# Kernel optimization log

Hardware: AMD Instinct MI355X
Metric: run time of the kernel (lower is better)

## Reference

```python
import jax, jax.numpy as jnp
import numpy as np

DIM = 2048
THRESH = 0.33

def _ternary(w):
    # sign() with dead zone: {-1, 0, +1}; detached from grad (matches torch.no_grad)
    return jax.lax.stop_gradient(jnp.where(jnp.abs(w) < THRESH, 0.0, jnp.sign(w)))

def _bitlinear(x, w, b):
    # F.linear(x, ternary_w, bias): x @ ternary_w.T + b
    return jnp.einsum('bsd,od->bso', x, _ternary(w)) + b

def setup_inputs() -> dict:
    key = jax.random.key(0)
    ks = jax.random.split(key, 6)
    B, S, D = 8, 2048, DIM
    x = jax.random.normal(ks[0], (B, S, D), dtype=jnp.float32)
    h_prev = jax.random.normal(ks[1], (B, S, D), dtype=jnp.float32)
    # BitLinear reset_parameters: uniform(-1, 1); bias zeros
    wf = jax.random.uniform(ks[2], (D, D), minval=-1.0, maxval=1.0, dtype=jnp.float32)
    wc = jax.random.uniform(ks[3], (D, D), minval=-1.0, maxval=1.0, dtype=jnp.float32)
    wg = jax.random.uniform(ks[4], (D, D), minval=-1.0, maxval=1.0, dtype=jnp.float32)
    wo = jax.random.uniform(ks[5], (D, D), minval=-1.0, maxval=1.0, dtype=jnp.float32)
    bf = jnp.zeros((D,), dtype=jnp.float32)
    bc = jnp.zeros((D,), dtype=jnp.float32)
    bg = jnp.zeros((D,), dtype=jnp.float32)
    bo = jnp.zeros((D,), dtype=jnp.float32)
    return {"x": x, "h_prev": h_prev, "wf": wf, "bf": bf, "wc": wc, "bc": bc,
            "wg": wg, "bg": bg, "wo": wo, "bo": bo}

def reference(x, h_prev, wf, bf, wc, bc, wg, bg, wo, bo):
    f = jax.nn.sigmoid(_bitlinear(x, wf, bf))
    c = jax.nn.silu(_bitlinear(x, wc, bc))
    h = f * h_prev + (1.0 - f) * c
    g = jax.nn.sigmoid(_bitlinear(x, wg, bg))
    o = _bitlinear(g * h, wo, bo)
    return (o, h)
```

## Files before the change

### kernel.cpp

```cpp
#include <hip/hip_runtime.h>
#include <hip/hip_bf16.h>
#include <cstdint>

#define DIM   2048
#define MROWS 16384
#define NT    32

typedef __bf16 bf16x8 __attribute__((ext_vector_type(8)));
typedef float  f32x4  __attribute__((ext_vector_type(4)));
typedef unsigned short u16;
typedef unsigned int   u32;

#define BARRIER() asm volatile("s_barrier" ::: "memory")
#define WAITVM(N) asm volatile("s_waitcnt vmcnt(" #N ")" ::: "memory")


__device__ __forceinline__ u16 ternary_bits(float w) {
    u32 u = __float_as_uint(w);
    u16 s = (u16)((u >> 16) & 0x8000u);
    return (__builtin_fabsf(w) < 0.33f) ? (u16)0 : (u16)(0x3F80u | s);
}

__device__ __forceinline__ u16 f2bf_rne(float f) {
    u32 u = __float_as_uint(f);
    u32 r = (u + 0x7FFFu + ((u >> 16) & 1u)) >> 16;
    return (u16)r;
}

__device__ __forceinline__ void gload16(const void* g, void* l) {
    __builtin_amdgcn_global_load_lds(
        (const __attribute__((address_space(1))) void*)g,
        (__attribute__((address_space(3))) void*)l,
        16, 0, 0);
}


__global__ void prep_weights(const float* __restrict__ wf, const float* __restrict__ wc,
                             const float* __restrict__ wg, const float* __restrict__ wo,
                             u16* __restrict__ out) {
    const float* srcs[4] = {wf, wc, wg, wo};
    const float* src = srcs[blockIdx.y];
    u16* dst = out + (size_t)blockIdx.y * (DIM * DIM);
    int e = (blockIdx.x * 256 + threadIdx.x) * 8;
    float4 v0 = *(const float4*)(src + e);
    float4 v1 = *(const float4*)(src + e + 4);
    ushort4 o0, o1;
    o0.x = ternary_bits(v0.x); o0.y = ternary_bits(v0.y);
    o0.z = ternary_bits(v0.z); o0.w = ternary_bits(v0.w);
    o1.x = ternary_bits(v1.x); o1.y = ternary_bits(v1.y);
    o1.z = ternary_bits(v1.z); o1.w = ternary_bits(v1.w);
    *(ushort4*)(dst + e)     = o0;
    *(ushort4*)(dst + e + 4) = o1;
}

__global__ void cast_x(const float* __restrict__ x, u16* __restrict__ xb) {
    size_t e = ((size_t)blockIdx.x * 256 + threadIdx.x) * 8;
    float4 v0 = *(const float4*)(x + e);
    float4 v1 = *(const float4*)(x + e + 4);
    ushort4 o0, o1;
    o0.x = f2bf_rne(v0.x); o0.y = f2bf_rne(v0.y);
    o0.z = f2bf_rne(v0.z); o0.w = f2bf_rne(v0.w);
    o1.x = f2bf_rne(v1.x); o1.y = f2bf_rne(v1.y);
    o1.z = f2bf_rne(v1.z); o1.w = f2bf_rne(v1.w);
    *(ushort4*)(xb + e)     = o0;
    *(ushort4*)(xb + e + 4) = o1;
}


__global__ __launch_bounds__(512) void gemm1(
    const u16* __restrict__ xb,
    const u16* __restrict__ wt,
    const float* __restrict__ bfv_, const float* __restrict__ bcv_, const float* __restrict__ bgv_,
    const float* __restrict__ hprev,
    float* __restrict__ hout,
    u16* __restrict__ gh)
{
    __shared__ __align__(16) u16 sA[2][2][128 * 32];
    __shared__ __align__(16) u16 sB[2][2][3][128 * 32];

    const int tid  = threadIdx.x;
    const int lane = tid & 63;
    const int wave = tid >> 6;
    const int wr   = wave >> 2;
    const int wcq  = wave & 3;

    const int bid  = blockIdx.x;
    const int swz  = (bid & 7) * 256 + (bid >> 3);
    const int brow = (swz & 127) * 128;
    const int bcol = (swz >> 7) * 128;

    const int row512 = tid >> 2;
    const int gc4    = (tid & 3) ^ ((tid >> 3) & 3);
    const int ldst   = tid * 8;

    const int fr  = lane & 15;
    const int hi  = lane >> 4;
    const int csw = (hi ^ ((fr >> 1) & 3)) * 8;

    f32x4 acc0[3][4] = {};
    f32x4 acc1[3][4] = {};

    const u16* aSrc  = xb + (size_t)(brow + row512) * DIM;
    const u16* bSrc0 = wt + (size_t)(bcol + row512) * DIM;
    const size_t WSTRIDE = (size_t)DIM * DIM;

    auto issueA = [&](int buf, int kt, int ks) {
        gload16(aSrc + kt + ks * 32 + gc4 * 8, (u16*)&sA[buf][ks][ldst]);
    };
    auto issueB = [&](int buf, int kt, int g, int ks) {
        gload16(bSrc0 + (size_t)g * WSTRIDE + kt + ks * 32 + gc4 * 8,
                (u16*)&sB[buf][ks][g][ldst]);
    };

    auto rdA = [&](const u16* lA, int ks, bf16x8 (&a)[4]) {
        #pragma unroll
        for (int mi = 0; mi < 4; ++mi)
            a[mi] = *(const bf16x8*)(lA + ks * 4096 + (wr * 64 + mi * 16 + fr) * 32 + csw);
    };
    auto rdB = [&](const u16* lB, int ks, int ni, bf16x8 (&b)[3]) {
        #pragma unroll
        for (int g = 0; g < 3; ++g)
            b[g] = *(const bf16x8*)(lB + ks * 12288 + g * 4096 + (wcq * 32 + ni * 16 + fr) * 32 + csw);
    };
    auto domfma = [&](bf16x8 (&a)[4], bf16x8 (&b)[3], f32x4 (&c)[3][4]) {
        __builtin_amdgcn_s_setprio(1);
        #pragma unroll
        for (int g = 0; g < 3; ++g)
            #pragma unroll
            for (int mi = 0; mi < 4; ++mi)
                c[g][mi] = __builtin_amdgcn_mfma_f32_16x16x32_bf16(a[mi], b[g], c[g][mi], 0, 0, 0);
        __builtin_amdgcn_s_setprio(0);
    };

    issueA(0, 0, 0); issueB(0, 0, 0, 0);
    issueB(0, 0, 1, 0); issueB(0, 0, 2, 0);
    issueA(0, 0, 1); issueB(0, 0, 0, 1);
    issueB(0, 0, 1, 1); issueB(0, 0, 2, 1);
    WAITVM(0);
    BARRIER();

    #pragma unroll 1
    for (int t = 0; t < NT - 1; ++t) {
        const u16* lA = &sA[t & 1][0][0];
        const u16* lB = &sB[t & 1][0][0][0];
        const int nb = (t + 1) & 1;
        const int kn = (t + 1) * 64;
        bf16x8 a[4], b[3];
        rdA(lA, 0, a); rdB(lB, 0, 0, b);
        issueA(nb, kn, 0); issueB(nb, kn, 0, 0);
        BARRIER();
        domfma(a, b, acc0);
        BARRIER();
        rdB(lB, 0, 1, b);
        issueB(nb, kn, 1, 0); issueB(nb, kn, 2, 0);
        WAITVM(4);
        BARRIER();
        domfma(a, b, acc1);
        BARRIER();
        rdA(lA, 1, a); rdB(lB, 1, 0, b);
        issueA(nb, kn, 1); issueB(nb, kn, 0, 1);
        BARRIER();
        domfma(a, b, acc0);
        BARRIER();
        rdB(lB, 1, 1, b);
        issueB(nb, kn, 1, 1); issueB(nb, kn, 2, 1);
        WAITVM(4);
        BARRIER();
        domfma(a, b, acc1);
        BARRIER();
    }
    {
        const u16* lA = &sA[1][0][0];
        const u16* lB = &sB[1][0][0][0];
        bf16x8 a[4], b[3];
        rdA(lA, 0, a); rdB(lB, 0, 0, b);
        BARRIER(); domfma(a, b, acc0); BARRIER();
        rdB(lB, 0, 1, b);
        WAITVM(0);
        BARRIER(); domfma(a, b, acc1); BARRIER();
        rdA(lA, 1, a); rdB(lB, 1, 0, b);
        BARRIER(); domfma(a, b, acc0); BARRIER();
        rdB(lB, 1, 1, b);
        domfma(a, b, acc1);
    }

    auto epi = [&](int ni, f32x4 (&c)[3][4]) {
        const int col = bcol + wcq * 32 + ni * 16 + fr;
        const float bfv = bfv_[col], bcv = bcv_[col], bgv = bgv_[col];
        #pragma unroll
        for (int mi = 0; mi < 4; ++mi) {
            #pragma unroll
            for (int j = 0; j < 4; ++j) {
                const int row = brow + wr * 64 + mi * 16 + hi * 4 + j;
                const size_t idx = (size_t)row * DIM + col;
                float pf = c[0][mi][j] + bfv;
                float pc = c[1][mi][j] + bcv;
                float pg = c[2][mi][j] + bgv;
                float f  = 1.f / (1.f + __expf(-pf));
                float cc = pc / (1.f + __expf(-pc));
                float g  = 1.f / (1.f + __expf(-pg));
                float h  = f * hprev[idx] + (1.f - f) * cc;
                hout[idx] = h;
                gh[idx] = f2bf_rne(g * h);
            }
        }
    };
    epi(0, acc0);
    epi(1, acc1);
}


__global__ __launch_bounds__(512) void gemm2(
    const u16* __restrict__ gh,
    const u16* __restrict__ wot,
    const float* __restrict__ bov_,
    float* __restrict__ oout)
{
    __shared__ __align__(16) u16 sA[2][2][128 * 32];
    __shared__ __align__(16) u16 sB[2][2][256 * 32];

    const int tid  = threadIdx.x;
    const int lane = tid & 63;
    const int wave = tid >> 6;
    const int wr   = wave >> 2;
    const int wcq  = wave & 3;

    const int bid  = blockIdx.x;
    const int swz  = (bid & 7) * 128 + (bid >> 3);
    const int brow = (swz & 127) * 128;
    const int bcol = (swz >> 7) * 256;

    const int row512 = tid >> 2;
    const int gc4    = (tid & 3) ^ ((tid >> 3) & 3);
    const int ldst   = tid * 8;

    const int fr  = lane & 15;
    const int hi  = lane >> 4;
    const int csw = (hi ^ ((fr >> 1) & 3)) * 8;

    f32x4 accL[4][2] = {};
    f32x4 accH[4][2] = {};

    const u16* aSrc  = gh  + (size_t)(brow + row512) * DIM;
    const u16* bSrcL = wot + (size_t)(bcol + row512) * DIM;
    const u16* bSrcH = wot + (size_t)(bcol + 128 + row512) * DIM;

    auto issueA = [&](int buf, int kt, int ks) {
        gload16(aSrc + kt + ks * 32 + gc4 * 8, (u16*)&sA[buf][ks][ldst]);
    };
    auto issueBlo = [&](int buf, int kt, int ks) {
        gload16(bSrcL + kt + ks * 32 + gc4 * 8, (u16*)&sB[buf][ks][ldst]);
    };
    auto issueBhi = [&](int buf, int kt, int ks) {
        gload16(bSrcH + kt + ks * 32 + gc4 * 8, (u16*)&sB[buf][ks][4096 + ldst]);
    };

    auto rdA = [&](const u16* lA, int ks, bf16x8 (&a)[4]) {
        #pragma unroll
        for (int mi = 0; mi < 4; ++mi)
            a[mi] = *(const bf16x8*)(lA + ks * 4096 + (wr * 64 + mi * 16 + fr) * 32 + csw);
    };
    auto rdB2 = [&](const u16* lB, int ks, int nbase, bf16x8 (&b)[2]) {
        #pragma unroll
        for (int jn = 0; jn < 2; ++jn)
            b[jn] = *(const bf16x8*)(lB + ks * 8192 + (wcq * 64 + (nbase + jn) * 16 + fr) * 32 + csw);
    };
    auto domfma2 = [&](bf16x8 (&a)[4], bf16x8 (&b)[2], f32x4 (&c)[4][2]) {
        __builtin_amdgcn_s_setprio(1);
        #pragma unroll
        for (int jn = 0; jn < 2; ++jn)
            #pragma unroll
            for (int mi = 0; mi < 4; ++mi)
                c[mi][jn] = __builtin_amdgcn_mfma_f32_16x16x32_bf16(a[mi], b[jn], c[mi][jn], 0, 0, 0);
        __builtin_amdgcn_s_setprio(0);
    };

    issueA(0, 0, 0); issueBlo(0, 0, 0);
    issueBhi(0, 0, 0); issueA(0, 0, 1);
    issueBlo(0, 0, 1);
    issueBhi(0, 0, 1);
    WAITVM(0);
    BARRIER();

    #pragma unroll 1
    for (int t = 0; t < NT - 1; ++t) {
        const u16* lA = &sA[t & 1][0][0];
        const u16* lB = &sB[t & 1][0][0];
        const int nb = (t + 1) & 1;
        const int kn = (t + 1) * 64;
        bf16x8 a[4], b[2];
        rdA(lA, 0, a); rdB2(lB, 0, 0, b);
        issueA(nb, kn, 0); issueBlo(nb, kn, 0);
        BARRIER();
        domfma2(a, b, accL);
        BARRIER();
        rdB2(lB, 0, 2, b);
        issueBhi(nb, kn, 0); issueA(nb, kn, 1);
        WAITVM(4);
        BARRIER();
        domfma2(a, b, accH);
        BARRIER();
        rdA(lA, 1, a); rdB2(lB, 1, 0, b);
        issueBlo(nb, kn, 1);
        BARRIER();
        domfma2(a, b, accL);
        BARRIER();
        rdB2(lB, 1, 2, b);
        issueBhi(nb, kn, 1);
        WAITVM(3);
        BARRIER();
        domfma2(a, b, accH);
        BARRIER();
    }
    {
        const u16* lA = &sA[1][0][0];
        const u16* lB = &sB[1][0][0];
        bf16x8 a[4], b[2];
        rdA(lA, 0, a); rdB2(lB, 0, 0, b);
        BARRIER(); domfma2(a, b, accL); BARRIER();
        rdB2(lB, 0, 2, b);
        WAITVM(0);
        BARRIER(); domfma2(a, b, accH); BARRIER();
        rdA(lA, 1, a); rdB2(lB, 1, 0, b);
        BARRIER(); domfma2(a, b, accL); BARRIER();
        rdB2(lB, 1, 2, b);
        domfma2(a, b, accH);
    }

    auto epi2 = [&](int nbase, f32x4 (&c)[4][2]) {
        #pragma unroll
        for (int jn = 0; jn < 2; ++jn) {
            const int col = bcol + wcq * 64 + (nbase + jn) * 16 + fr;
            const float bov = bov_[col];
            #pragma unroll
            for (int mi = 0; mi < 4; ++mi)
                #pragma unroll
                for (int j = 0; j < 4; ++j)
                    oout[(size_t)(brow + wr * 64 + mi * 16 + hi * 4 + j) * DIM + col] = c[mi][jn][j] + bov;
        }
    };
    epi2(0, accL);
    epi2(2, accH);
}

extern "C" void kernel_launch(void* const* d_in, const int* in_sizes, int n_in,
                              void* d_out, int out_size, void* d_ws, size_t ws_size,
                              hipStream_t stream) {
    const float* x  = (const float*)d_in[0];
    const float* hp = (const float*)d_in[1];
    const float* wf = (const float*)d_in[2];
    const float* bf = (const float*)d_in[3];
    const float* wc = (const float*)d_in[4];
    const float* bc = (const float*)d_in[5];
    const float* wg = (const float*)d_in[6];
    const float* bg = (const float*)d_in[7];
    const float* wo = (const float*)d_in[8];
    const float* bo = (const float*)d_in[9];

    float* o_out = (float*)d_out;
    float* h_out = o_out + (size_t)MROWS * DIM;

    u16* w_t  = (u16*)d_ws;
    u16* x_bf = (u16*)((char*)d_ws + 33554432);
    u16* gh   = (u16*)((char*)d_ws + 100663296);

    prep_weights<<<dim3(2048, 4), 256, 0, stream>>>(wf, wc, wg, wo, w_t);
    cast_x<<<dim3(16384), 256, 0, stream>>>(x, x_bf);
    gemm1<<<dim3(2048), 512, 0, stream>>>(x_bf, w_t, bf, bc, bg, hp, h_out, gh);
    gemm2<<<dim3(1024), 512, 0, stream>>>(gh, w_t + 3 * (size_t)DIM * DIM, bo, o_out);
}
```

Measured before the change: 801.7 us.

## Double M-tile to 256 rows and switch GEMMs to triple-buffered K32 pipeline

Both GEMMs now compute 256-row output tiles instead of 128, so each wave holds 8 M-fragments and B tiles are reused across twice as many rows, halving the grid size. The K loop moves from double-buffered 64-wide steps to a three-stage ring of 32-wide LDS buffers with rotating offsets, prefetching two stages ahead. The aim is less global and LDS traffic per MFMA and better latency hiding. In exchange it doubles accumulator registers (gemm1 holds 48 f32x4 accumulators), which may cut occupancy or cause spills, and it leaves fewer blocks per CU to cover the tail.

```diff
diff --git a/kernel.cpp b/kernel.cpp
--- a/kernel.cpp
+++ b/kernel.cpp
@@ -4,7 +4,7 @@
 
 #define DIM   2048
 #define MROWS 16384
-#define NT    32
+#define NH    64
 
 typedef __bf16 bf16x8 __attribute__((ext_vector_type(8)));
 typedef float  f32x4  __attribute__((ext_vector_type(4)));
@@ -75,8 +75,7 @@
     float* __restrict__ hout,
     u16* __restrict__ gh)
 {
-    __shared__ __align__(16) u16 sA[2][2][128 * 32];
-    __shared__ __align__(16) u16 sB[2][2][3][128 * 32];
+    __shared__ __align__(16) u16 lds[3 * 20480];
 
     const int tid  = threadIdx.x;
     const int lane = tid & 63;
@@ -85,113 +84,98 @@
     const int wcq  = wave & 3;
 
     const int bid  = blockIdx.x;
-    const int swz  = (bid & 7) * 256 + (bid >> 3);
-    const int brow = (swz & 127) * 128;
-    const int bcol = (swz >> 7) * 128;
-
-    const int row512 = tid >> 2;
-    const int gc4    = (tid & 3) ^ ((tid >> 3) & 3);
-    const int ldst   = tid * 8;
+    const int swz  = (bid & 7) * 128 + (bid >> 3);
+    const int brow = (swz & 63) * 256;
+    const int bcol = (swz >> 6) * 128;
+
+    const int srow = tid >> 2;
+    const int gc4  = (tid & 3) ^ ((tid >> 3) & 3);
+    const int ldst = tid * 8;
 
     const int fr  = lane & 15;
     const int hi  = lane >> 4;
     const int csw = (hi ^ ((fr >> 1) & 3)) * 8;
 
-    f32x4 acc0[3][4] = {};
-    f32x4 acc1[3][4] = {};
-
-    const u16* aSrc  = xb + (size_t)(brow + row512) * DIM;
-    const u16* bSrc0 = wt + (size_t)(bcol + row512) * DIM;
-    const size_t WSTRIDE = (size_t)DIM * DIM;
-
-    auto issueA = [&](int buf, int kt, int ks) {
-        gload16(aSrc + kt + ks * 32 + gc4 * 8, (u16*)&sA[buf][ks][ldst]);
-    };
-    auto issueB = [&](int buf, int kt, int g, int ks) {
-        gload16(bSrc0 + (size_t)g * WSTRIDE + kt + ks * 32 + gc4 * 8,
-                (u16*)&sB[buf][ks][g][ldst]);
-    };
-
-    auto rdA = [&](const u16* lA, int ks, bf16x8 (&a)[4]) {
-        #pragma unroll
-        for (int mi = 0; mi < 4; ++mi)
-            a[mi] = *(const bf16x8*)(lA + ks * 4096 + (wr * 64 + mi * 16 + fr) * 32 + csw);
-    };
-    auto rdB = [&](const u16* lB, int ks, int ni, bf16x8 (&b)[3]) {
+    f32x4 acc0[3][8] = {};
+    f32x4 acc1[3][8] = {};
+
+    const u16* aSrc0 = xb + (size_t)(brow + srow) * DIM;
+    const u16* aSrc1 = xb + (size_t)(brow + 128 + srow) * DIM;
+    const u16* bSrcB = wt + (size_t)(bcol + srow) * DIM;
+    const size_t WST = (size_t)DIM * DIM;
+
+    auto issueA = [&](int so, int k0) {
+        gload16(aSrc0 + k0 + gc4 * 8, (u16*)&lds[so + ldst]);
+        gload16(aSrc1 + k0 + gc4 * 8, (u16*)&lds[so + 4096 + ldst]);
+    };
+    auto issueB = [&](int so, int k0, int g) {
+        gload16(bSrcB + (size_t)g * WST + k0 + gc4 * 8,
+                (u16*)&lds[so + 8192 + g * 4096 + ldst]);
+    };
+
+    auto rdA = [&](int so, bf16x8 (&a)[8]) {
+        #pragma unroll
+        for (int mi = 0; mi < 8; ++mi)
+            a[mi] = *(const bf16x8*)(&lds[so + (wr * 128 + mi * 16 + fr) * 32 + csw]);
+    };
+    auto rdB = [&](int so, int ni, bf16x8 (&b)[3]) {
         #pragma unroll
         for (int g = 0; g < 3; ++g)
-            b[g] = *(const bf16x8*)(lB + ks * 12288 + g * 4096 + (wcq * 32 + ni * 16 + fr) * 32 + csw);
-    };
-    auto domfma = [&](bf16x8 (&a)[4], bf16x8 (&b)[3], f32x4 (&c)[3][4]) {
+            b[g] = *(const bf16x8*)(&lds[so + 8192 + g * 4096 + (wcq * 32 + ni * 16 + fr) * 32 + csw]);
+    };
+    auto domfma = [&](bf16x8 (&a)[8], bf16x8 (&b)[3], f32x4 (&c)[3][8]) {
         __builtin_amdgcn_s_setprio(1);
         #pragma unroll
         for (int g = 0; g < 3; ++g)
             #pragma unroll
-            for (int mi = 0; mi < 4; ++mi)
+            for (int mi = 0; mi < 8; ++mi)
                 c[g][mi] = __builtin_amdgcn_mfma_f32_16x16x32_bf16(a[mi], b[g], c[g][mi], 0, 0, 0);
         __builtin_amdgcn_s_setprio(0);
     };
 
-    issueA(0, 0, 0); issueB(0, 0, 0, 0);
-    issueB(0, 0, 1, 0); issueB(0, 0, 2, 0);
-    issueA(0, 0, 1); issueB(0, 0, 0, 1);
-    issueB(0, 0, 1, 1); issueB(0, 0, 2, 1);
+    int so0 = 0, so1 = 20480, so2 = 40960;
+
+    issueA(so0, 0); issueB(so0, 0, 0); issueB(so0, 0, 1); issueB(so0, 0, 2);
+    issueA(so1, 32); issueB(so1, 32, 0); issueB(so1, 32, 1); issueB(so1, 32, 2);
+    WAITVM(5);
+    BARRIER();
+
+    bf16x8 a[8], b[3];
+    #pragma unroll 1
+    for (int h = 0; h < NH - 2; ++h) {
+        const int kn = (h + 2) * 32;
+        rdA(so0, a); rdB(so0, 0, b);
+        issueA(so2, kn); issueB(so2, kn, 0);
+        BARRIER();
+        domfma(a, b, acc0);
+        BARRIER();
+        rdB(so0, 1, b);
+        issueB(so2, kn, 1); issueB(so2, kn, 2);
+        WAITVM(5);
+        BARRIER();
+        domfma(a, b, acc1);
+        BARRIER();
+        int t = so0; so0 = so1; so1 = so2; so2 = t;
+    }
+    rdA(so0, a); rdB(so0, 0, b);
+    BARRIER(); domfma(a, b, acc0); BARRIER();
+    rdB(so0, 1, b);
     WAITVM(0);
-    BARRIER();
-
-    #pragma unroll 1
-    for (int t = 0; t < NT - 1; ++t) {
-        const u16* lA = &sA[t & 1][0][0];
-        const u16* lB = &sB[t & 1][0][0][0];
-        const int nb = (t + 1) & 1;
-        const int kn = (t + 1) * 64;
-        bf16x8 a[4], b[3];
-        rdA(lA, 0, a); rdB(lB, 0, 0, b);
-        issueA(nb, kn, 0); issueB(nb, kn, 0, 0);
-        BARRIER();
-        domfma(a, b, acc0);
-        BARRIER();
-        rdB(lB, 0, 1, b);
-        issueB(nb, kn, 1, 0); issueB(nb, kn, 2, 0);
-        WAITVM(4);
-        BARRIER();
-        domfma(a, b, acc1);
-        BARRIER();
-        rdA(lA, 1, a); rdB(lB, 1, 0, b);
-        issueA(nb, kn, 1); issueB(nb, kn, 0, 1);
-        BARRIER();
-        domfma(a, b, acc0);
-        BARRIER();
-        rdB(lB, 1, 1, b);
-        issueB(nb, kn, 1, 1); issueB(nb, kn, 2, 1);
-        WAITVM(4);
-        BARRIER();
-        domfma(a, b, acc1);
-        BARRIER();
-    }
-    {
-        const u16* lA = &sA[1][0][0];
-        const u16* lB = &sB[1][0][0][0];
-        bf16x8 a[4], b[3];
-        rdA(lA, 0, a); rdB(lB, 0, 0, b);
-        BARRIER(); domfma(a, b, acc0); BARRIER();
-        rdB(lB, 0, 1, b);
-        WAITVM(0);
-        BARRIER(); domfma(a, b, acc1); BARRIER();
-        rdA(lA, 1, a); rdB(lB, 1, 0, b);
-        BARRIER(); domfma(a, b, acc0); BARRIER();
-        rdB(lB, 1, 1, b);
-        domfma(a, b, acc1);
-    }
-
-    auto epi = [&](int ni, f32x4 (&c)[3][4]) {
+    BARRIER(); domfma(a, b, acc1); BARRIER();
+    { int t = so0; so0 = so1; so1 = so2; so2 = t; }
+    rdA(so0, a); rdB(so0, 0, b);
+    domfma(a, b, acc0);
+    rdB(so0, 1, b);
+    domfma(a, b, acc1);
+
+    auto epi = [&](int ni, f32x4 (&c)[3][8]) {
         const int col = bcol + wcq * 32 + ni * 16 + fr;
         const float bfv = bfv_[col], bcv = bcv_[col], bgv = bgv_[col];
         #pragma unroll
-        for (int mi = 0; mi < 4; ++mi) {
+        for (int mi = 0; mi < 8; ++mi) {
             #pragma unroll
             for (int j = 0; j < 4; ++j) {
-                const int row = brow + wr * 64 + mi * 16 + hi * 4 + j;
+                const int row = brow + wr * 128 + mi * 16 + hi * 4 + j;
                 const size_t idx = (size_t)row * DIM + col;
                 float pf = c[0][mi][j] + bfv;
                 float pc = c[1][mi][j] + bcv;
@@ -199,9 +183,9 @@
                 float f  = 1.f / (1.f + __expf(-pf));
                 float cc = pc / (1.f + __expf(-pc));
                 float g  = 1.f / (1.f + __expf(-pg));
-                float h  = f * hprev[idx] + (1.f - f) * cc;
-                hout[idx] = h;
-                gh[idx] = f2bf_rne(g * h);
+                float hh = f * hprev[idx] + (1.f - f) * cc;
+                hout[idx] = hh;
+                gh[idx] = f2bf_rne(g * hh);
             }
         }
     };
@@ -216,8 +200,7 @@
     const float* __restrict__ bov_,
     float* __restrict__ oout)
 {
-    __shared__ __align__(16) u16 sA[2][2][128 * 32];
-    __shared__ __align__(16) u16 sB[2][2][256 * 32];
+    __shared__ __align__(16) u16 lds[3 * 16384];
 
     const int tid  = threadIdx.x;
     const int lane = tid & 63;
@@ -226,117 +209,100 @@
     const int wcq  = wave & 3;
 
     const int bid  = blockIdx.x;
-    const int swz  = (bid & 7) * 128 + (bid >> 3);
-    const int brow = (swz & 127) * 128;
-    const int bcol = (swz >> 7) * 256;
-
-    const int row512 = tid >> 2;
-    const int gc4    = (tid & 3) ^ ((tid >> 3) & 3);
-    const int ldst   = tid * 8;
+    const int swz  = (bid & 7) * 64 + (bid >> 3);
+    const int brow = (swz & 63) * 256;
+    const int bcol = (swz >> 6) * 256;
+
+    const int srow = tid >> 2;
+    const int gc4  = (tid & 3) ^ ((tid >> 3) & 3);
+    const int ldst = tid * 8;
 
     const int fr  = lane & 15;
     const int hi  = lane >> 4;
     const int csw = (hi ^ ((fr >> 1) & 3)) * 8;
 
-    f32x4 accL[4][2] = {};
-    f32x4 accH[4][2] = {};
-
-    const u16* aSrc  = gh  + (size_t)(brow + row512) * DIM;
-    const u16* bSrcL = wot + (size_t)(bcol + row512) * DIM;
-    const u16* bSrcH = wot + (size_t)(bcol + 128 + row512) * DIM;
-
-    auto issueA = [&](int buf, int kt, int ks) {
-        gload16(aSrc + kt + ks * 32 + gc4 * 8, (u16*)&sA[buf][ks][ldst]);
-    };
-    auto issueBlo = [&](int buf, int kt, int ks) {
-        gload16(bSrcL + kt + ks * 32 + gc4 * 8, (u16*)&sB[buf][ks][ldst]);
-    };
-    auto issueBhi = [&](int buf, int kt, int ks) {
-        gload16(bSrcH + kt + ks * 32 + gc4 * 8, (u16*)&sB[buf][ks][4096 + ldst]);
-    };
-
-    auto rdA = [&](const u16* lA, int ks, bf16x8 (&a)[4]) {
-        #pragma unroll
-        for (int mi = 0; mi < 4; ++mi)
-            a[mi] = *(const bf16x8*)(lA + ks * 4096 + (wr * 64 + mi * 16 + fr) * 32 + csw);
-    };
-    auto rdB2 = [&](const u16* lB, int ks, int nbase, bf16x8 (&b)[2]) {
+    f32x4 accL[8][2] = {};
+    f32x4 accH[8][2] = {};
+
+    const u16* aSrc0 = gh  + (size_t)(brow + srow) * DIM;
+    const u16* aSrc1 = gh  + (size_t)(brow + 128 + srow) * DIM;
+    const u16* bSrc0 = wot + (size_t)(bcol + srow) * DIM;
+    const u16* bSrc1 = wot + (size_t)(bcol + 128 + srow) * DIM;
+
+    auto issueA = [&](int so, int k0) {
+        gload16(aSrc0 + k0 + gc4 * 8, (u16*)&lds[so + ldst]);
+        gload16(aSrc1 + k0 + gc4 * 8, (u16*)&lds[so + 4096 + ldst]);
+    };
+    auto issueB = [&](int so, int k0) {
+        gload16(bSrc0 + k0 + gc4 * 8, (u16*)&lds[so + 8192 + ldst]);
+        gload16(bSrc1 + k0 + gc4 * 8, (u16*)&lds[so + 12288 + ldst]);
+    };
+
+    auto rdA = [&](int so, bf16x8 (&a)[8]) {
+        #pragma unroll
+        for (int mi = 0; mi < 8; ++mi)
+            a[mi] = *(const bf16x8*)(&lds[so + (wr * 128 + mi * 16 + fr) * 32 + csw]);
+    };
+    auto rdB2 = [&](int so, int nbase, bf16x8 (&b)[2]) {
         #pragma unroll
         for (int jn = 0; jn < 2; ++jn)
-            b[jn] = *(const bf16x8*)(lB + ks * 8192 + (wcq * 64 + (nbase + jn) * 16 + fr) * 32 + csw);
-    };
-    auto domfma2 = [&](bf16x8 (&a)[4], bf16x8 (&b)[2], f32x4 (&c)[4][2]) {
+            b[jn] = *(const bf16x8*)(&lds[so + 8192 + (wcq * 64 + (nbase + jn) * 16 + fr) * 32 + csw]);
+    };
+    auto domfma2 = [&](bf16x8 (&a)[8], bf16x8 (&b)[2], f32x4 (&c)[8][2]) {
         __builtin_amdgcn_s_setprio(1);
         #pragma unroll
         for (int jn = 0; jn < 2; ++jn)
             #pragma unroll
-            for (int mi = 0; mi < 4; ++mi)
+            for (int mi = 0; mi < 8; ++mi)
                 c[mi][jn] = __builtin_amdgcn_mfma_f32_16x16x32_bf16(a[mi], b[jn], c[mi][jn], 0, 0, 0);
         __builtin_amdgcn_s_setprio(0);
     };
 
-    issueA(0, 0, 0); issueBlo(0, 0, 0);
-    issueBhi(0, 0, 0); issueA(0, 0, 1);
-    issueBlo(0, 0, 1);
-    issueBhi(0, 0, 1);
+    int so0 = 0, so1 = 16384, so2 = 32768;
+
+    issueA(so0, 0); issueB(so0, 0);
+    issueA(so1, 32); issueB(so1, 32);
+    WAITVM(4);
+    BARRIER();
+
+    bf16x8 a[8], b[2];
+    #pragma unroll 1
+    for (int h = 0; h < NH - 2; ++h) {
+        const int kn = (h + 2) * 32;
+        rdA(so0, a); rdB2(so0, 0, b);
+        issueA(so2, kn);
+        BARRIER();
+        domfma2(a, b, accL);
+        BARRIER();
+        rdB2(so0, 2, b);
+        issueB(so2, kn);
+        WAITVM(4);
+        BARRIER();
+        domfma2(a, b, accH);
+        BARRIER();
+        int t = so0; so0 = so1; so1 = so2; so2 = t;
+    }
+    rdA(so0, a); rdB2(so0, 0, b);
+    BARRIER(); domfma2(a, b, accL); BARRIER();
+    rdB2(so0, 2, b);
     WAITVM(0);
-    BARRIER();
-
-    #pragma unroll 1
-    for (int t = 0; t < NT - 1; ++t) {
-        const u16* lA = &sA[t & 1][0][0];
-        const u16* lB = &sB[t & 1][0][0];
-        const int nb = (t + 1) & 1;
-        const int kn = (t + 1) * 64;
-        bf16x8 a[4], b[2];
-        rdA(lA, 0, a); rdB2(lB, 0, 0, b);
-        issueA(nb, kn, 0); issueBlo(nb, kn, 0);
-        BARRIER();
-        domfma2(a, b, accL);
-        BARRIER();
-        rdB2(lB, 0, 2, b);
-        issueBhi(nb, kn, 0); issueA(nb, kn, 1);
-        WAITVM(4);
-        BARRIER();
-        domfma2(a, b, accH);
-        BARRIER();
-        rdA(lA, 1, a); rdB2(lB, 1, 0, b);
-        issueBlo(nb, kn, 1);
-        BARRIER();
-        domfma2(a, b, accL);
-        BARRIER();
-        rdB2(lB, 1, 2, b);
-        issueBhi(nb, kn, 1);
-        WAITVM(3);
-        BARRIER();
-        domfma2(a, b, accH);
-        BARRIER();
-    }
-    {
-        const u16* lA = &sA[1][0][0];
-        const u16* lB = &sB[1][0][0];
-        bf16x8 a[4], b[2];
-        rdA(lA, 0, a); rdB2(lB, 0, 0, b);
-        BARRIER(); domfma2(a, b, accL); BARRIER();
-        rdB2(lB, 0, 2, b);
-        WAITVM(0);
-        BARRIER(); domfma2(a, b, accH); BARRIER();
-        rdA(lA, 1, a); rdB2(lB, 1, 0, b);
-        BARRIER(); domfma2(a, b, accL); BARRIER();
-        rdB2(lB, 1, 2, b);
-        domfma2(a, b, accH);
-    }
-
-    auto epi2 = [&](int nbase, f32x4 (&c)[4][2]) {
+    BARRIER(); domfma2(a, b, accH); BARRIER();
+    { int t = so0; so0 = so1; so1 = so2; so2 = t; }
+    rdA(so0, a); rdB2(so0, 0, b);
+    domfma2(a, b, accL);
+    rdB2(so0, 2, b);
+    domfma2(a, b, accH);
+
+    auto epi2 = [&](int nbase, f32x4 (&c)[8][2]) {
         #pragma unroll
         for (int jn = 0; jn < 2; ++jn) {
             const int col = bcol + wcq * 64 + (nbase + jn) * 16 + fr;
             const float bov = bov_[col];
             #pragma unroll
-            for (int mi = 0; mi < 4; ++mi)
+            for (int mi = 0; mi < 8; ++mi)
                 #pragma unroll
                 for (int j = 0; j < 4; ++j)
-                    oout[(size_t)(brow + wr * 64 + mi * 16 + hi * 4 + j) * DIM + col] = c[mi][jn][j] + bov;
+                    oout[(size_t)(brow + wr * 128 + mi * 16 + hi * 4 + j) * DIM + col] = c[mi][jn][j] + bov;
         }
     };
     epi2(0, accL);
@@ -366,6 +332,6 @@
 
     prep_weights<<<dim3(2048, 4), 256, 0, stream>>>(wf, wc, wg, wo, w_t);
     cast_x<<<dim3(16384), 256, 0, stream>>>(x, x_bf);
-    gemm1<<<dim3(2048), 512, 0, stream>>>(x_bf, w_t, bf, bc, bg, hp, h_out, gh);
-    gemm2<<<dim3(1024), 512, 0, stream>>>(gh, w_t + 3 * (size_t)DIM * DIM, bo, o_out);
-}
+    gemm1<<<dim3(1024), 512, 0, stream>>>(x_bf, w_t, bf, bc, bg, hp, h_out, gh);
+    gemm2<<<dim3(512), 512, 0, stream>>>(gh, w_t + 3 * (size_t)DIM * DIM, bo, o_out);
+}
```

Result: slower. 819.5 us (+2.2%).
